# Optimization experiments

Measured on AMD Instinct MI355X. Metric: run time of the kernel, lower is better.

## Reference

```python
import jax, jax.numpy as jnp
import numpy as np


def _layernorm(x, w, b, eps=1e-5):
    mu = x.mean(-1, keepdims=True)
    var = ((x - mu) ** 2).mean(-1, keepdims=True)
    return (x - mu) / jnp.sqrt(var + eps) * w + b


def _conv_res3d(x, w, b):
    # Conv3d(k=3, pad=1) + InstanceNorm3d (no affine) + LeakyReLU(0.01), residual add
    y = jax.lax.conv_general_dilated(x, w, (1, 1, 1), 'SAME',
                                     dimension_numbers=('NCDHW', 'OIDHW', 'NCDHW'))
    y = y + b[None, :, None, None, None]
    mu = y.mean((2, 3, 4), keepdims=True)
    var = ((y - mu) ** 2).mean((2, 3, 4), keepdims=True)
    y = (y - mu) / jnp.sqrt(var + 1e-5)
    y = jnp.where(y >= 0, y, 0.01 * y)
    return x + y


def _ssm(xl, delta_w, delta_b, Bp_w, Cp_w, A_log):
    # xl: [n, l, d_inner]; selective scan with lax.scan over l
    A = -jax.nn.softplus(A_log)                                   # [d_state], broadcast over d_inner
    delta = jnp.clip(jax.nn.softplus(xl @ delta_w.T + delta_b), 1e-4, 10.0)
    Bm = xl @ Bp_w.T                                              # [n, l, d_state]
    Cm = xl @ Cp_w.T
    n, l, di = xl.shape
    ds = A_log.shape[0]

    def step(h, inp):
        d_t, x_t, b_t, c_t = inp                                  # [n,di],[n,di],[n,ds],[n,ds]
        A_bar = jnp.exp(d_t[:, :, None] * A)                      # [n,di,ds]
        h = A_bar * h + (d_t * x_t)[:, :, None] * b_t[:, None, :]
        y = jnp.einsum('nds,ns->nd', h, c_t)
        return h, y

    h0 = jnp.zeros((n, di, ds), xl.dtype)
    _, ys = jax.lax.scan(step, h0, (jnp.swapaxes(delta, 0, 1), jnp.swapaxes(xl, 0, 1),
                                    jnp.swapaxes(Bm, 0, 1), jnp.swapaxes(Cm, 0, 1)))
    return jnp.swapaxes(ys, 0, 1)                                 # [n, l, d_inner]


def _mamba(x, p):
    # x: [n, l, d_model] (already layer-normed)
    left = x @ p['left_w'].T                                      # [n, l, d_inner]
    left = jnp.swapaxes(left, 1, 2)                               # [n, d_inner, l]
    dc = p['conv1d_w'].shape[-1]
    left = jnp.pad(left, ((0, 0), (0, 0), (dc - 1, 0)))           # causal pad
    left = jax.lax.conv_general_dilated(left, p['conv1d_w'], (1,), 'VALID',
                                        feature_group_count=p['conv1d_w'].shape[0],
                                        dimension_numbers=('NCH', 'OIH', 'NCH'))
    left = left + p['conv1d_b'][None, :, None]
    left = jax.nn.silu(jnp.swapaxes(left, 1, 2))                  # [n, l, d_inner]
    y = _ssm(left, p['delta_w'], p['delta_b'], p['Bp_w'], p['Cp_w'], p['A_log'])
    gate = jax.nn.silu(x @ p['right_w'].T)
    out = _layernorm(y * gate, p['pn_w'], p['pn_b'])
    return out @ p['out_w'].T                                     # [n, l, d_model]


def reference(x, cr1_w, cr1_b, cr2_w, cr2_b, ln_w, ln_b, left_w, conv1d_w, conv1d_b,
              delta_w, delta_b, Bp_w, Cp_w, A_log, right_w, pn_w, pn_b, out_w,
              res_scale, axis_w):
    p = dict(left_w=left_w, conv1d_w=conv1d_w, conv1d_b=conv1d_b, delta_w=delta_w,
             delta_b=delta_b, Bp_w=Bp_w, Cp_w=Cp_w, A_log=A_log, right_w=right_w,
             pn_w=pn_w, pn_b=pn_b, out_w=out_w)
    identity = x
    B, C, H, W, D = x.shape
    x = _conv_res3d(x, cr1_w, cr1_b)
    x = _conv_res3d(x, cr2_w, cr2_b)

    xh = jnp.transpose(x, (0, 3, 4, 2, 1)).reshape(B * W * D, H, C)
    mh = _mamba(_layernorm(xh, ln_w, ln_b), p).reshape(B, W, D, H, C).transpose(0, 4, 3, 1, 2)

    xw = jnp.transpose(x, (0, 2, 4, 3, 1)).reshape(B * H * D, W, C)
    mw = _mamba(_layernorm(xw, ln_w, ln_b), p).reshape(B, H, D, W, C).transpose(0, 4, 1, 3, 2)

    xd = jnp.transpose(x, (0, 2, 3, 4, 1)).reshape(B * H * W, D, C)
    md = _mamba(_layernorm(xd, ln_w, ln_b), p).reshape(B, H, W, D, C).transpose(0, 4, 1, 2, 3)

    w = jax.nn.softmax(axis_w)
    out = w[0] * mh + w[1] * mw + w[2] * md
    return identity + res_scale * out


def setup_inputs() -> dict:
    key = jax.random.key(0)
    ks = jax.random.split(key, 12)
    B, C, H, W, D = 2, 64, 32, 32, 32
    ds, dc = 16, 4
    di = 2 * C
    f32 = jnp.float32

    def xav(k, shape):
        fan_in, fan_out = shape[-1], shape[0]
        return jax.random.normal(k, shape, f32) * np.sqrt(2.0 / (fan_in + fan_out))

    return {
        'x': jax.random.normal(ks[0], (B, C, H, W, D), f32),
        'cr1_w': jax.random.normal(ks[1], (C, C, 3, 3, 3), f32) / np.sqrt(C * 27),
        'cr1_b': jnp.zeros((C,), f32),
        'cr2_w': jax.random.normal(ks[2], (C, C, 3, 3, 3), f32) / np.sqrt(C * 27),
        'cr2_b': jnp.zeros((C,), f32),
        'ln_w': jnp.ones((C,), f32),
        'ln_b': jnp.zeros((C,), f32),
        'left_w': xav(ks[3], (di, C)),
        'conv1d_w': jax.random.normal(ks[4], (di, 1, dc), f32) / np.sqrt(dc),
        'conv1d_b': jnp.zeros((di,), f32),
        'delta_w': jax.random.normal(ks[5], (di, di), f32) / np.sqrt(di),
        'delta_b': jnp.zeros((di,), f32),
        'Bp_w': jax.random.normal(ks[6], (ds, di), f32) / np.sqrt(di),
        'Cp_w': jax.random.normal(ks[7], (ds, di), f32) / np.sqrt(di),
        'A_log': jnp.log(jnp.arange(1, ds + 1, dtype=f32)),
        'right_w': xav(ks[8], (di, C)),
        'pn_w': jnp.ones((di,), f32),
        'pn_b': jnp.zeros((di,), f32),
        'out_w': xav(ks[9], (C, di)),
        'res_scale': jnp.asarray(0.1, f32),
        'axis_w': jnp.zeros((3,), f32),
    }
```

## Files before the change

### kernel.cpp

```cpp
#include <hip/hip_runtime.h>
#include <hip/hip_bf16.h>
#include <math.h>
#include <stdint.h>


typedef __attribute__((ext_vector_type(8))) short short8;
typedef __attribute__((ext_vector_type(4))) float f32x4;
typedef __attribute__((ext_vector_type(2))) float f32x2;

__device__ __forceinline__ float siluf(float x){ return x * (1.0f / (1.0f + __expf(-x))); }
__device__ __forceinline__ float softplusf(float x){ return fmaxf(x, 0.0f) + log1pf(__expf(-fabsf(x))); }
__device__ __forceinline__ float softplus_hw(float x){
  float t = __builtin_amdgcn_exp2f(-fabsf(x) * 1.44269504088896f);
  return fmaxf(x, 0.0f) + 0.69314718055995f * __builtin_amdgcn_logf(1.0f + t);
}
__device__ __forceinline__ float b2f(short s){
  unsigned int u = ((unsigned int)(unsigned short)s) << 16;
  float f; __builtin_memcpy(&f, &u, 4); return f;
}
__device__ __forceinline__ short f2b(float v){
  __hip_bfloat16 h = __float2bfloat16(v);
  unsigned short u; __builtin_memcpy(&u, &h, 2); return (short)u;
}
__device__ __forceinline__ f32x2 bf2x(unsigned int u){
  unsigned int lo = u << 16;
  unsigned int hi = u & 0xffff0000u;
  float fl, fh;
  __builtin_memcpy(&fl, &lo, 4);
  __builtin_memcpy(&fh, &hi, 4);
  return (f32x2){fl, fh};
}

__device__ __forceinline__ void gld_lds16(const void* g, void* l){
  __builtin_amdgcn_global_load_lds(
      (__attribute__((address_space(1))) void*)(uintptr_t)g,
      (__attribute__((address_space(3))) void*)(uint32_t)(uintptr_t)l,
      16, 0, 0);
}

__global__ __launch_bounds__(256) void setup_k(uint4* __restrict__ xz,
    const float* __restrict__ cr1w, const float* __restrict__ cr2w,
    const float* __restrict__ lw, const float* __restrict__ rwt,
    const float* __restrict__ dwt, const float* __restrict__ bw,
    const float* __restrict__ cwp, const float* __restrict__ owt,
    const float* __restrict__ alog,
    __hip_bfloat16* __restrict__ W4a, __hip_bfloat16* __restrict__ W4b,
    __hip_bfloat16* __restrict__ Wlr, __hip_bfloat16* __restrict__ Wd,
    __hip_bfloat16* __restrict__ oWp, float* __restrict__ negA2,
    uint4* __restrict__ statz)
{
  int i = blockIdx.x * 256 + threadIdx.x;
  if (i < 628864){ uint4 z; z.x = z.y = z.z = z.w = 0u; xz[i] = z; return; }
  i -= 628864;
  if (i < 110592){
    int tap = i >> 12, co = (i >> 6) & 63, ci = i & 63;
    W4a[i] = __float2bfloat16(cr1w[(co * 64 + ci) * 27 + tap]); return;
  }
  i -= 110592;
  if (i < 110592){
    int tap = i >> 12, co = (i >> 6) & 63, ci = i & 63;
    W4b[i] = __float2bfloat16(cr2w[(co * 64 + ci) * 27 + tap]); return;
  }
  i -= 110592;
  if (i < 16384){
    int row = i >> 6, c = i & 63;
    float v = (row < 128) ? lw[row * 64 + c] : rwt[(row - 128) * 64 + c];
    Wlr[i] = __float2bfloat16(v); return;
  }
  i -= 16384;
  if (i < 20480){
    int row = i >> 7, k = i & 127;
    float v = (row < 128) ? dwt[row * 128 + k]
            : (row < 144 ? bw[(row - 128) * 128 + k] : cwp[(row - 144) * 128 + k]);
    Wd[i] = __float2bfloat16(v); return;
  }
  i -= 20480;
  if (i < 8192){ oWp[i] = __float2bfloat16(owt[i]); return; }
  i -= 8192;
  if (i < 16){ negA2[i] = -softplusf(alog[i]) * 1.44269504088896f; return; }
  i -= 16;
  if (i < 128){ uint4 z; z.x = z.y = z.z = z.w = 0u; statz[i] = z; return; }
}

__global__ __launch_bounds__(256) void pack_k(const float* __restrict__ xin,
                                              __hip_bfloat16* __restrict__ xpad)
{
  __shared__ float lds[64 * 33];
  const int t = threadIdx.x, blk = blockIdx.x;
  const int b = blk >> 10, h = (blk >> 5) & 31, w = blk & 31;
  const size_t rbase = ((size_t)(b * 64) << 15) + h * 1024 + w * 32;
  #pragma unroll
  for (int r = 0; r < 8; r++){
    int c = r * 8 + (t >> 5), d = t & 31;
    lds[c * 33 + d] = xin[rbase + (size_t)c * 32768 + d];
  }
  __syncthreads();
  const size_t wbase = (size_t)b * 2515456 + (size_t)(h + 1) * 73984 + (w + 1) * 2176 + 64;
  #pragma unroll
  for (int r = 0; r < 8; r++){
    int d = r * 4 + (t >> 6), c = t & 63;
    xpad[wbase + d * 64 + c] = __float2bfloat16(lds[c * 33 + d]);
  }
}

__global__ __launch_bounds__(256) void conv_mfma_k(const __hip_bfloat16* __restrict__ xpad,
    const __hip_bfloat16* __restrict__ W4, __hip_bfloat16* __restrict__ y,
    float* __restrict__ stats)
{
  __shared__ short smem[24576];

  const int t = threadIdx.x;
  const int wave = t >> 6, lane = t & 63;
  const int quad = lane >> 4, ln = lane & 15;

  const int blk = blockIdx.x;
  const int xcd = blk & 7, j = blk >> 3;
  const int b = j >> 5, jj = j & 31;
  const int h = xcd * 4 + (jj >> 3);
  const int w0 = (jj & 7) * 4;

  const int bcol = (lane >> 2) * 64 + (lane & 3) * 8;
  const __hip_bfloat16* Bg = xpad + (size_t)b * 2515456 + (size_t)h * 73984
                                  + (size_t)(w0 + wave) * 2176 + bcol;
  const __hip_bfloat16* Ag = W4 + wave * 1024 + bcol;

  f32x4 acc[2][4];
  #pragma unroll
  for (int jn = 0; jn < 2; jn++)
    #pragma unroll
    for (int m = 0; m < 4; m++) acc[jn][m] = (f32x4){0.f, 0.f, 0.f, 0.f};

  const int aoff = ln * 32 + quad * 8;
  const int boffl = wave * 2048 + ln * 32 + quad * 8;

  {
    short* S = &smem[0];
    gld_lds16(Bg,              S + wave * 2048);
    gld_lds16(Bg + 1024,       S + wave * 2048 + 512);
    gld_lds16(Bg + 32,         S + wave * 2048 + 1024);
    gld_lds16(Bg + 1024 + 32,  S + wave * 2048 + 1536);
    gld_lds16(Ag,              S + 8192 + wave * 512);
    gld_lds16(Ag + 32,         S + 8192 + 2048 + wave * 512);
  }
  int cur = 0;
  for (int t1 = 0; t1 < 27; t1++){
    __syncthreads();
    if (t1 + 1 < 27){
      const int t2 = t1 + 1;
      const int ki = t2 / 9, kj = (t2 / 3) % 3, kk = t2 % 3;
      const int tapoff = ki * 73984 + kj * 2176 + kk * 64;
      short* S = &smem[(cur ^ 1) * 12288];
      gld_lds16(Bg + tapoff,             S + wave * 2048);
      gld_lds16(Bg + tapoff + 1024,      S + wave * 2048 + 512);
      gld_lds16(Bg + tapoff + 32,        S + wave * 2048 + 1024);
      gld_lds16(Bg + tapoff + 1024 + 32, S + wave * 2048 + 1536);
      gld_lds16(Ag + t2 * 4096,          S + 8192 + wave * 512);
      gld_lds16(Ag + t2 * 4096 + 32,     S + 8192 + 2048 + wave * 512);
    }
    const int sb = cur * 12288;
    {
      short8 a0 = *(const short8*)&smem[sb + 8192 + aoff];
      short8 a1 = *(const short8*)&smem[sb + 8192 + 512 + aoff];
      short8 a2 = *(const short8*)&smem[sb + 8192 + 1024 + aoff];
      short8 a3 = *(const short8*)&smem[sb + 8192 + 1536 + aoff];
      short8 b0 = *(const short8*)&smem[sb + boffl];
      short8 b1 = *(const short8*)&smem[sb + boffl + 512];
      acc[0][0] = __builtin_amdgcn_mfma_f32_16x16x32_bf16(a0, b0, acc[0][0], 0, 0, 0);
      acc[0][1] = __builtin_amdgcn_mfma_f32_16x16x32_bf16(a1, b0, acc[0][1], 0, 0, 0);
      acc[0][2] = __builtin_amdgcn_mfma_f32_16x16x32_bf16(a2, b0, acc[0][2], 0, 0, 0);
      acc[0][3] = __builtin_amdgcn_mfma_f32_16x16x32_bf16(a3, b0, acc[0][3], 0, 0, 0);
      acc[1][0] = __builtin_amdgcn_mfma_f32_16x16x32_bf16(a0, b1, acc[1][0], 0, 0, 0);
      acc[1][1] = __builtin_amdgcn_mfma_f32_16x16x32_bf16(a1, b1, acc[1][1], 0, 0, 0);
      acc[1][2] = __builtin_amdgcn_mfma_f32_16x16x32_bf16(a2, b1, acc[1][2], 0, 0, 0);
      acc[1][3] = __builtin_amdgcn_mfma_f32_16x16x32_bf16(a3, b1, acc[1][3], 0, 0, 0);
    }
    {
      short8 a0 = *(const short8*)&smem[sb + 8192 + 2048 + aoff];
      short8 a1 = *(const short8*)&smem[sb + 8192 + 2048 + 512 + aoff];
      short8 a2 = *(const short8*)&smem[sb + 8192 + 2048 + 1024 + aoff];
      short8 a3 = *(const short8*)&smem[sb + 8192 + 2048 + 1536 + aoff];
      short8 b0 = *(const short8*)&smem[sb + boffl + 1024];
      short8 b1 = *(const short8*)&smem[sb + boffl + 1536];
      acc[0][0] = __builtin_amdgcn_mfma_f32_16x16x32_bf16(a0, b0, acc[0][0], 0, 0, 0);
      acc[0][1] = __builtin_amdgcn_mfma_f32_16x16x32_bf16(a1, b0, acc[0][1], 0, 0, 0);
      acc[0][2] = __builtin_amdgcn_mfma_f32_16x16x32_bf16(a2, b0, acc[0][2], 0, 0, 0);
      acc[0][3] = __builtin_amdgcn_mfma_f32_16x16x32_bf16(a3, b0, acc[0][3], 0, 0, 0);
      acc[1][0] = __builtin_amdgcn_mfma_f32_16x16x32_bf16(a0, b1, acc[1][0], 0, 0, 0);
      acc[1][1] = __builtin_amdgcn_mfma_f32_16x16x32_bf16(a1, b1, acc[1][1], 0, 0, 0);
      acc[1][2] = __builtin_amdgcn_mfma_f32_16x16x32_bf16(a2, b1, acc[1][2], 0, 0, 0);
      acc[1][3] = __builtin_amdgcn_mfma_f32_16x16x32_bf16(a3, b1, acc[1][3], 0, 0, 0);
    }
    cur ^= 1;
  }

  const size_t sbase = (size_t)h * 1024 + (w0 + wave) * 32 + ln;
  #pragma unroll
  for (int jn = 0; jn < 2; jn++){
    #pragma unroll
    for (int mt = 0; mt < 4; mt++){
      #pragma unroll
      for (int reg = 0; reg < 4; reg++){
        int co = mt * 16 + quad * 4 + reg;
        y[(((size_t)(b * 64 + co)) << 15) + sbase + jn * 16] = __float2bfloat16(acc[jn][mt][reg]);
      }
    }
  }

  __syncthreads();
  float* sred = (float*)smem;
  #pragma unroll
  for (int mt = 0; mt < 4; mt++){
    #pragma unroll
    for (int reg = 0; reg < 4; reg++){
      float a0 = acc[0][mt][reg], a1 = acc[1][mt][reg];
      float s = a0 + a1, s2 = a0 * a0 + a1 * a1;
      #pragma unroll
      for (int m = 1; m < 16; m <<= 1){
        s  += __shfl_xor(s, m);
        s2 += __shfl_xor(s2, m);
      }
      if (ln == 0){
        const int idx = (((wave * 4 + quad) * 4 + mt) * 4 + reg) * 2;
        sred[idx] = s; sred[idx + 1] = s2;
      }
    }
  }
  __syncthreads();
  if (t < 128){
    const int k = t & 1, reg = (t >> 1) & 3, mt = (t >> 3) & 3, q = t >> 5;
    float v = 0.f;
    #pragma unroll
    for (int wv = 0; wv < 4; wv++)
      v += sred[(((wv * 4 + q) * 4 + mt) * 4 + reg) * 2 + k];
    const int co = mt * 16 + q * 4 + reg;
    atomicAdd(&stats[k * 128 + b * 64 + co], v);
  }
}

__global__ __launch_bounds__(256) void apply_pack_k(const float* __restrict__ xin,
    const __hip_bfloat16* __restrict__ y, const float* __restrict__ stats,
    __hip_bfloat16* __restrict__ x1b, __hip_bfloat16* __restrict__ xpad)
{
  __shared__ float lds[64 * 33];
  const int t = threadIdx.x, blk = blockIdx.x;
  const int b = blk >> 10, h = (blk >> 5) & 31, w = blk & 31;
  const size_t rbase = ((size_t)(b * 64) << 15) + h * 1024 + w * 32;
  const int c = t >> 2, d0 = (t & 3) * 8;
  const float s1v = stats[b * 64 + c], s2v = stats[128 + b * 64 + c];
  const float mu = s1v * (1.0f / 32768.0f);
  const float var = s2v * (1.0f / 32768.0f) - mu * mu;
  const float rs = rsqrtf(fmaxf(var, 0.f) + 1e-5f);
  const size_t idx = rbase + (size_t)c * 32768 + d0;
  short8 yv = *(const short8*)&y[idx];
  float4 xa = *(const float4*)&xin[idx];
  float4 xb = *(const float4*)&xin[idx + 4];
  short8 o;
  #pragma unroll
  for (int jj = 0; jj < 8; jj++){
    float v = (b2f(yv[jj]) - mu) * rs;
    v = (v >= 0.0f) ? v : 0.01f * v;
    v += (jj < 4) ? ((const float*)&xa)[jj] : ((const float*)&xb)[jj - 4];
    o[jj] = f2b(v);
    lds[c * 33 + d0 + jj] = v;
  }
  *(short8*)&x1b[idx] = o;
  __syncthreads();
  const size_t wbase = (size_t)b * 2515456 + (size_t)(h + 1) * 73984 + (w + 1) * 2176 + 64;
  #pragma unroll
  for (int r = 0; r < 8; r++){
    int d = r * 4 + (t >> 6), cc = t & 63;
    xpad[wbase + d * 64 + cc] = __float2bfloat16(lds[cc * 33 + d]);
  }
}

__global__ __launch_bounds__(256) void ln_lr_k(const __hip_bfloat16* __restrict__ x1b,
    const __hip_bfloat16* __restrict__ y, const float* __restrict__ stats,
    const float* __restrict__ lnw, const float* __restrict__ lnb,
    const __hip_bfloat16* __restrict__ Wlr, __hip_bfloat16* __restrict__ Lb,
    __hip_bfloat16* __restrict__ Gb)
{
  __shared__ float lds_v[2][64 * 33];
  __shared__ float s_mu[64], s_rs[64];
  __shared__ short s_ln[64 * 68];

  const int t = threadIdx.x, blk = blockIdx.x;
  const int b = blk >> 9;
  const int h = (blk >> 4) & 31;
  const int w0 = (blk & 15) * 2;

  const int c = t >> 2, d0 = (t & 3) * 8;
  const float s1v = stats[b * 64 + c], s2v = stats[128 + b * 64 + c];
  const float mu0 = s1v * (1.0f / 32768.0f);
  const float var0 = s2v * (1.0f / 32768.0f) - mu0 * mu0;
  const float rs0 = rsqrtf(fmaxf(var0, 0.f) + 1e-5f);
  #pragma unroll
  for (int wl = 0; wl < 2; wl++){
    const size_t rbase = ((size_t)(b * 64) << 15) + h * 1024 + (w0 + wl) * 32;
    const size_t idx = rbase + (size_t)c * 32768 + d0;
    short8 yv = *(const short8*)&y[idx];
    short8 xv = *(const short8*)&x1b[idx];
    #pragma unroll
    for (int jj = 0; jj < 8; jj++){
      float v = (b2f(yv[jj]) - mu0) * rs0;
      v = (v >= 0.0f) ? v : 0.01f * v;
      lds_v[wl][c * 33 + d0 + jj] = v + b2f(xv[jj]);
    }
  }
  __syncthreads();

  if (t < 64){
    const int wl = t >> 5, d = t & 31;
    float s = 0.f, s2 = 0.f;
    for (int cc = 0; cc < 64; cc++){
      float v = lds_v[wl][cc * 33 + d];
      s += v; s2 += v * v;
    }
    float mu = s * (1.f / 64.f);
    float var = s2 * (1.f / 64.f) - mu * mu;
    s_mu[t] = mu; s_rs[t] = rsqrtf(var + 1e-5f);
  }
  __syncthreads();

  {
    const int pos_loc = t >> 2, c0 = (t & 3) * 16;
    const int wl = pos_loc >> 5, d = pos_loc & 31;
    const float mu = s_mu[pos_loc], rs = s_rs[pos_loc];
    #pragma unroll
    for (int k = 0; k < 16; k++){
      const int cc = c0 + k;
      s_ln[pos_loc * 68 + cc] = f2b((lds_v[wl][cc * 33 + d] - mu) * rs * lnw[cc] + lnb[cc]);
    }
  }
  __syncthreads();

  const int wave = t >> 6, lane = t & 63, quad = lane >> 4, ln = lane & 15;
  const int pos0 = blk * 64 + wave * 16;
  f32x4 acc[16];
  #pragma unroll
  for (int nt = 0; nt < 16; nt++) acc[nt] = (f32x4){0.f, 0.f, 0.f, 0.f};
  #pragma unroll
  for (int ks = 0; ks < 2; ks++){
    short8 a = *(const short8*)&s_ln[(wave * 16 + ln) * 68 + ks * 32 + quad * 8];
    #pragma unroll
    for (int nt = 0; nt < 16; nt++){
      short8 bv = *(const short8*)&Wlr[(nt * 16 + ln) * 64 + ks * 32 + quad * 8];
      acc[nt] = __builtin_amdgcn_mfma_f32_16x16x32_bf16(a, bv, acc[nt], 0, 0, 0);
    }
  }
  #pragma unroll
  for (int nt = 0; nt < 16; nt++){
    int col = nt * 16 + ln;
    #pragma unroll
    for (int reg = 0; reg < 4; reg++){
      int pos = pos0 + quad * 4 + reg;
      float v = acc[nt][reg];
      if (col < 128) Lb[(size_t)pos * 128 + col] = __float2bfloat16(v);
      else           Gb[(size_t)pos * 128 + col - 128] = __float2bfloat16(siluf(v));
    }
  }
}

__global__ __launch_bounds__(256) void dbcscan_k(const __hip_bfloat16* __restrict__ Lb,
    const float* __restrict__ cw, const float* __restrict__ cb,
    const __hip_bfloat16* __restrict__ Wd, const float* __restrict__ db,
    const __hip_bfloat16* __restrict__ Gb, const float* __restrict__ negA2,
    const float* __restrict__ pnw, const float* __restrict__ pnb,
    const float* __restrict__ axw,
    __hip_bfloat16* __restrict__ Y0, __hip_bfloat16* __restrict__ Y1,
    __hip_bfloat16* __restrict__ Y2)
{
  __shared__ short s_xl[64 * 136];
  __shared__ short s_d[64 * 128];
  __shared__ short s_Bh[2][32][16];
  __shared__ short s_Ch[2][32][16];
  __shared__ float s_stat[2][32][2];

  const int t = threadIdx.x;
  const int bid = blockIdx.x;
  const int axis = bid % 3;
  const int j = bid / 3;
  int sigma;
  if (axis == 0)      sigma = 1024;
  else if (axis == 1) sigma = 32;
  else                sigma = 1;
  __hip_bfloat16* Yax = (axis == 0) ? Y0 : (axis == 1) ? Y1 : Y2;

  int bases[2];
  #pragma unroll
  for (int s = 0; s < 2; s++){
    const int seq = j * 2 + s;
    const int b = seq >> 10, r1 = (seq >> 5) & 31, r0 = seq & 31;
    if (axis == 0)      bases[s] = b * 32768 + r1 * 32 + r0;
    else if (axis == 1) bases[s] = b * 32768 + r1 * 1024 + r0;
    else                bases[s] = b * 32768 + r1 * 1024 + r0 * 32;
  }

  {
    const int c0 = (t & 15) * 8;
    const int pibase = t >> 4;
    float4 w4[8]; float cbv[8];
    #pragma unroll
    for (int c = 0; c < 8; c++){ w4[c] = *(const float4*)&cw[(c0 + c) * 4]; cbv[c] = cb[c0 + c]; }
    #pragma unroll
    for (int r = 0; r < 4; r++){
      const int row = pibase + r * 16;
      const int sl_ = row >> 5, l = row & 31;
      const int pos = bases[sl_] + l * sigma;
      float acc[8];
      #pragma unroll
      for (int c = 0; c < 8; c++) acc[c] = cbv[c];
      #pragma unroll
      for (int jt = 0; jt < 4; jt++){
        const int off = 3 - jt;
        if (l >= off){
          short8 lv = *(const short8*)&Lb[(size_t)(pos - off * sigma) * 128 + c0];
          #pragma unroll
          for (int c = 0; c < 8; c++){
            float wv = (jt == 0) ? w4[c].x : (jt == 1) ? w4[c].y : (jt == 2) ? w4[c].z : w4[c].w;
            acc[c] += wv * b2f(lv[c]);
          }
        }
      }
      short8 o;
      #pragma unroll
      for (int c = 0; c < 8; c++) o[c] = f2b(siluf(acc[c]));
      *(short8*)&s_xl[row * 136 + c0] = o;
    }
  }
  __syncthreads();

  const int wave = t >> 6, lane = t & 63, quad = lane >> 4, ln = lane & 15;
  {
    const int rowb = (wave * 16 + ln) * 136;
    f32x4 acc2[10];
    #pragma unroll
    for (int nt = 0; nt < 10; nt++) acc2[nt] = (f32x4){0.f, 0.f, 0.f, 0.f};
    #pragma unroll
    for (int ks = 0; ks < 4; ks++){
      short8 a = *(const short8*)&s_xl[rowb + ks * 32 + quad * 8];
      #pragma unroll
      for (int nt = 0; nt < 10; nt++){
        short8 bv = *(const short8*)&Wd[(nt * 16 + ln) * 128 + ks * 32 + quad * 8];
        acc2[nt] = __builtin_amdgcn_mfma_f32_16x16x32_bf16(a, bv, acc2[nt], 0, 0, 0);
      }
    }
    const int row0 = wave * 16 + quad * 4;
    #pragma unroll
    for (int nt = 0; nt < 10; nt++){
      const int col = nt * 16 + ln;
      const bool isd = col < 128;
      const float dbv = isd ? db[col] : 0.f;
      #pragma unroll
      for (int reg = 0; reg < 4; reg++){
        const int row = row0 + reg;
        float v = acc2[nt][reg];
        if (isd){
          v = fminf(fmaxf(softplus_hw(v + dbv), 1e-4f), 10.f);
          s_d[row * 128 + col] = f2b(v);
        } else {
          const int sl_ = row >> 5, l = row & 31, cc = col - 128;
          if (cc < 16) s_Bh[sl_][l][cc] = f2b(v);
          else         s_Ch[sl_][l][cc - 16] = f2b(v);
        }
      }
    }
  }

  f32x2 A22[8], h2[8];
  #pragma unroll
  for (int s = 0; s < 8; s++){
    A22[s] = (f32x2){negA2[2 * s], negA2[2 * s + 1]};
    h2[s] = (f32x2){0.f, 0.f};
  }
  const int sl = wave >> 1;
  const int half = wave & 1;
  const int ch = half * 64 + lane;
  const int base = bases[sl];
  const size_t sx = (size_t)sigma * 128;
  const __hip_bfloat16* pg = Gb + (size_t)base * 128 + ch;

  __syncthreads();

  unsigned short gu = *(const unsigned short*)pg;
  #pragma unroll
  for (int l = 0; l < 32; l++){
    unsigned short ngu = 0;
    if (l + 1 < 32) ngu = *(const unsigned short*)(pg + sx);
    const int row = sl * 32 + l;
    float dt = b2f(s_d[row * 128 + ch]);
    float xt = b2f(s_xl[row * 136 + ch]);
    float g = b2f((short)gu);
    float dx = dt * xt;
    const f32x2 dt2 = (f32x2){dt, dt};
    const f32x2 dx2 = (f32x2){dx, dx};
    uint4 Bu0 = *(const uint4*)&s_Bh[sl][l][0];
    uint4 Bu1 = *(const uint4*)&s_Bh[sl][l][8];
    uint4 Cu0 = *(const uint4*)&s_Ch[sl][l][0];
    uint4 Cu1 = *(const uint4*)&s_Ch[sl][l][8];
    const unsigned int Bw[8] = {Bu0.x, Bu0.y, Bu0.z, Bu0.w, Bu1.x, Bu1.y, Bu1.z, Bu1.w};
    const unsigned int Cw[8] = {Cu0.x, Cu0.y, Cu0.z, Cu0.w, Cu1.x, Cu1.y, Cu1.z, Cu1.w};
    f32x2 y2 = (f32x2){0.f, 0.f};
    #pragma unroll
    for (int i = 0; i < 8; i++){
      f32x2 dtA = dt2 * A22[i];
      f32x2 es = (f32x2){__builtin_amdgcn_exp2f(dtA.x),
                         __builtin_amdgcn_exp2f(dtA.y)};
      h2[i] = es * h2[i] + dx2 * bf2x(Bw[i]);
      y2 = y2 + h2[i] * bf2x(Cw[i]);
    }
    float y = y2.x + y2.y;
    s_d[row * 128 + ch] = f2b(y * g);
    gu = ngu;
    pg += sx;
  }
  __syncthreads();

  {
    const int row = t >> 2, part = t & 3;
    const int sl2 = row >> 5, l2 = row & 31;
    const short* yr = &s_d[row * 128 + part * 32];
    float s1 = 0.f, s2 = 0.f;
    #pragma unroll
    for (int i = 0; i < 32; i++){
      float v = b2f(yr[i]);
      s1 += v; s2 += v * v;
    }
    s1 += __shfl_xor(s1, 1); s2 += __shfl_xor(s2, 1);
    s1 += __shfl_xor(s1, 2); s2 += __shfl_xor(s2, 2);
    if (part == 0){ s_stat[sl2][l2][0] = s1; s_stat[sl2][l2][1] = s2; }
  }
  __syncthreads();

  float a0 = axw[0], a1 = axw[1], a2 = axw[2];
  float mxw = fmaxf(a0, fmaxf(a1, a2));
  float e0 = __expf(a0 - mxw), e1 = __expf(a1 - mxw), e2 = __expf(a2 - mxw);
  float wax = ((axis == 0) ? e0 : (axis == 1) ? e1 : e2) / (e0 + e1 + e2);
  const float pw = pnw[ch], pb = pnb[ch];

  __hip_bfloat16* py = Yax + (size_t)base * 128 + ch;
  #pragma unroll
  for (int l = 0; l < 32; l++){
    float ss1 = s_stat[sl][l][0];
    float ss2 = s_stat[sl][l][1];
    float mu = ss1 * (1.f / 128.f);
    float var = ss2 * (1.f / 128.f) - mu * mu;
    float rs = rsqrtf(fmaxf(var, 0.f) + 1e-5f);
    float yv = b2f(s_d[(sl * 32 + l) * 128 + ch]);
    float o = ((yv - mu) * rs * pw + pb) * wax;
    *(unsigned short*)py = (unsigned short)f2b(o);
    py += sx;
  }
}

__global__ __launch_bounds__(256) void gemm_out_k(const __hip_bfloat16* __restrict__ Y0,
    const __hip_bfloat16* __restrict__ Y1, const __hip_bfloat16* __restrict__ Y2,
    const __hip_bfloat16* __restrict__ oW, const float* __restrict__ xres,
    const float* __restrict__ rsc, float* __restrict__ outp)
{
  const int t = threadIdx.x, wave = t >> 6, lane = t & 63, quad = lane >> 4, ln = lane & 15;
  const int pos0 = blockIdx.x * 64 + wave * 16;
  f32x4 acc[4];
  #pragma unroll
  for (int mt = 0; mt < 4; mt++) acc[mt] = (f32x4){0.f, 0.f, 0.f, 0.f};
  #pragma unroll
  for (int ks = 0; ks < 4; ks++){
    const size_t boffs = (size_t)(pos0 + ln) * 128 + ks * 32 + quad * 8;
    short8 bv0 = *(const short8*)&Y0[boffs];
    short8 bv1 = *(const short8*)&Y1[boffs];
    short8 bv2 = *(const short8*)&Y2[boffs];
    #pragma unroll
    for (int mt = 0; mt < 4; mt++){
      short8 a = *(const short8*)&oW[(mt * 16 + ln) * 128 + ks * 32 + quad * 8];
      acc[mt] = __builtin_amdgcn_mfma_f32_16x16x32_bf16(a, bv0, acc[mt], 0, 0, 0);
      acc[mt] = __builtin_amdgcn_mfma_f32_16x16x32_bf16(a, bv1, acc[mt], 0, 0, 0);
      acc[mt] = __builtin_amdgcn_mfma_f32_16x16x32_bf16(a, bv2, acc[mt], 0, 0, 0);
    }
  }
  float rs = rsc[0];
  const int pos = pos0 + ln;
  const int bb = pos >> 15, hwd = pos & 32767;
  #pragma unroll
  for (int mt = 0; mt < 4; mt++){
    #pragma unroll
    for (int reg = 0; reg < 4; reg++){
      int co = mt * 16 + quad * 4 + reg;
      size_t idx = (((size_t)(bb * 64 + co)) << 15) + hwd;
      outp[idx] = xres[idx] + rs * acc[mt][reg];
    }
  }
}

extern "C" void kernel_launch(void* const* d_in, const int* in_sizes, int n_in,
                              void* d_out, int out_size, void* d_ws, size_t ws_size,
                              hipStream_t stream)
{
  const float* x      = (const float*)d_in[0];
  const float* cr1w   = (const float*)d_in[1];
  const float* cr2w   = (const float*)d_in[3];
  const float* ln_w   = (const float*)d_in[5];
  const float* ln_b   = (const float*)d_in[6];
  const float* left_w = (const float*)d_in[7];
  const float* c1dw   = (const float*)d_in[8];
  const float* c1db   = (const float*)d_in[9];
  const float* dw     = (const float*)d_in[10];
  const float* db     = (const float*)d_in[11];
  const float* bpw    = (const float*)d_in[12];
  const float* cpw    = (const float*)d_in[13];
  const float* alog   = (const float*)d_in[14];
  const float* rw     = (const float*)d_in[15];
  const float* pnw    = (const float*)d_in[16];
  const float* pnb    = (const float*)d_in[17];
  const float* ow     = (const float*)d_in[18];
  const float* rsc    = (const float*)d_in[19];
  const float* axw    = (const float*)d_in[20];
  float* out = (float*)d_out;
  float* wsf = (float*)d_ws;

  __hip_bfloat16* ybuf = (__hip_bfloat16*)d_out;
  __hip_bfloat16* x1b  = (__hip_bfloat16*)wsf;
  float* stats1 = wsf + 4194304;
  float* stats2 = wsf + 4194560;
  float* negA2  = wsf + 4194816;
  __hip_bfloat16* W4a  = (__hip_bfloat16*)(wsf + 4195072);
  __hip_bfloat16* W4b  = W4a + 110592;
  __hip_bfloat16* Wlr  = (__hip_bfloat16*)(wsf + 4305664);
  __hip_bfloat16* Wdbc = (__hip_bfloat16*)(wsf + 4313856);
  __hip_bfloat16* oWp  = (__hip_bfloat16*)(wsf + 4324096);
  __hip_bfloat16* xpad = (__hip_bfloat16*)(wsf + 4328192);
  __hip_bfloat16* Lbuf = (__hip_bfloat16*)(wsf + 6843648);
  __hip_bfloat16* Gbuf = (__hip_bfloat16*)(wsf + 11037952);
  __hip_bfloat16* Y0   = (__hip_bfloat16*)wsf;
  __hip_bfloat16* Y1   = (__hip_bfloat16*)(wsf + 15232256);
  __hip_bfloat16* Y2   = (__hip_bfloat16*)(wsf + 19426560);

  setup_k<<<3498, 256, 0, stream>>>((uint4*)xpad, cr1w, cr2w, left_w, rw, dw, bpw, cpw, ow,
                                    alog, W4a, W4b, Wlr, Wdbc, oWp, negA2,
                                    (uint4*)stats1);

  pack_k<<<2048, 256, 0, stream>>>(x, xpad);
  conv_mfma_k<<<512, 256, 0, stream>>>(xpad, W4a, ybuf, stats1);
  apply_pack_k<<<2048, 256, 0, stream>>>(x, ybuf, stats1, x1b, xpad);
  conv_mfma_k<<<512, 256, 0, stream>>>(xpad, W4b, ybuf, stats2);
  ln_lr_k<<<1024, 256, 0, stream>>>(x1b, ybuf, stats2, ln_w, ln_b, Wlr, Lbuf, Gbuf);

  dbcscan_k<<<3072, 256, 0, stream>>>(Lbuf, c1dw, c1db, Wdbc, db, Gbuf, negA2,
                                      pnw, pnb, axw, Y0, Y1, Y2);

  gemm_out_k<<<1024, 256, 0, stream>>>(Y0, Y1, Y2, oWp, x, rsc, out);
}
```

Measured before the change: 389.8 us.

## Halve conv tile width and split output channels across waves

New measurement: 399.7 us. +2.5%, slower.

```diff
diff --git a/kernel.cpp b/kernel.cpp
--- a/kernel.cpp
+++ b/kernel.cpp
@@ -107,7 +107,7 @@
     const __hip_bfloat16* __restrict__ W4, __hip_bfloat16* __restrict__ y,
     float* __restrict__ stats)
 {
-  __shared__ short smem[24576];
+  __shared__ short smem[16384];
 
   const int t = threadIdx.x;
   const int wave = t >> 6, lane = t & 63;
@@ -115,32 +115,41 @@
 
   const int blk = blockIdx.x;
   const int xcd = blk & 7, j = blk >> 3;
-  const int b = j >> 5, jj = j & 31;
-  const int h = xcd * 4 + (jj >> 3);
-  const int w0 = (jj & 7) * 4;
+  const int b = j >> 6, jj = j & 63;
+  const int h = xcd * 4 + (jj >> 4);
+  const int w0 = (jj & 15) * 2;
+
+  const int wl = wave & 1;
+  const int coh = wave >> 1;
 
   const int bcol = (lane >> 2) * 64 + (lane & 3) * 8;
   const __hip_bfloat16* Bg = xpad + (size_t)b * 2515456 + (size_t)h * 73984
-                                  + (size_t)(w0 + wave) * 2176 + bcol;
-  const __hip_bfloat16* Ag = W4 + wave * 1024 + bcol;
-
-  f32x4 acc[2][4];
+                                  + (size_t)(w0 + (wave & 1)) * 2176 + bcol;
+  const __hip_bfloat16* Ag = W4 + (wave >= 2 ? (wave - 2) * 2048 : 0) + bcol;
+
+  f32x4 acc[2][2];
   #pragma unroll
   for (int jn = 0; jn < 2; jn++)
     #pragma unroll
-    for (int m = 0; m < 4; m++) acc[jn][m] = (f32x4){0.f, 0.f, 0.f, 0.f};
+    for (int m = 0; m < 2; m++) acc[jn][m] = (f32x4){0.f, 0.f, 0.f, 0.f};
 
   const int aoff = ln * 32 + quad * 8;
-  const int boffl = wave * 2048 + ln * 32 + quad * 8;
+  const int boff = wl * 2048 + ln * 32 + quad * 8;
 
   {
     short* S = &smem[0];
-    gld_lds16(Bg,              S + wave * 2048);
-    gld_lds16(Bg + 1024,       S + wave * 2048 + 512);
-    gld_lds16(Bg + 32,         S + wave * 2048 + 1024);
-    gld_lds16(Bg + 1024 + 32,  S + wave * 2048 + 1536);
-    gld_lds16(Ag,              S + 8192 + wave * 512);
-    gld_lds16(Ag + 32,         S + 8192 + 2048 + wave * 512);
+    if (wave < 2){
+      gld_lds16(Bg,             S + wave * 2048);
+      gld_lds16(Bg + 1024,      S + wave * 2048 + 512);
+      gld_lds16(Bg + 32,        S + wave * 2048 + 1024);
+      gld_lds16(Bg + 1024 + 32, S + wave * 2048 + 1536);
+    } else {
+      const int d0 = 4096 + (wave - 2) * 1024;
+      gld_lds16(Ag,         S + d0);
+      gld_lds16(Ag + 1024,  S + d0 + 512);
+      gld_lds16(Ag + 32,    S + d0 + 2048);
+      gld_lds16(Ag + 1056,  S + d0 + 2560);
+    }
   }
   int cur = 0;
   for (int t1 = 0; t1 < 27; t1++){
@@ -149,58 +158,52 @@
       const int t2 = t1 + 1;
       const int ki = t2 / 9, kj = (t2 / 3) % 3, kk = t2 % 3;
       const int tapoff = ki * 73984 + kj * 2176 + kk * 64;
-      short* S = &smem[(cur ^ 1) * 12288];
-      gld_lds16(Bg + tapoff,             S + wave * 2048);
-      gld_lds16(Bg + tapoff + 1024,      S + wave * 2048 + 512);
-      gld_lds16(Bg + tapoff + 32,        S + wave * 2048 + 1024);
-      gld_lds16(Bg + tapoff + 1024 + 32, S + wave * 2048 + 1536);
-      gld_lds16(Ag + t2 * 4096,          S + 8192 + wave * 512);
-      gld_lds16(Ag + t2 * 4096 + 32,     S + 8192 + 2048 + wave * 512);
-    }
-    const int sb = cur * 12288;
+      short* S = &smem[(cur ^ 1) * 8192];
+      if (wave < 2){
+        gld_lds16(Bg + tapoff,             S + wave * 2048);
+        gld_lds16(Bg + tapoff + 1024,      S + wave * 2048 + 512);
+        gld_lds16(Bg + tapoff + 32,        S + wave * 2048 + 1024);
+        gld_lds16(Bg + tapoff + 1024 + 32, S + wave * 2048 + 1536);
+      } else {
+        const int d0 = 4096 + (wave - 2) * 1024;
+        gld_lds16(Ag + t2 * 4096,        S + d0);
+        gld_lds16(Ag + t2 * 4096 + 1024, S + d0 + 512);
+        gld_lds16(Ag + t2 * 4096 + 32,   S + d0 + 2048);
+        gld_lds16(Ag + t2 * 4096 + 1056, S + d0 + 2560);
+      }
+    }
+    const int sb = cur * 8192;
     {
-      short8 a0 = *(const short8*)&smem[sb + 8192 + aoff];
-      short8 a1 = *(const short8*)&smem[sb + 8192 + 512 + aoff];
-      short8 a2 = *(const short8*)&smem[sb + 8192 + 1024 + aoff];
-      short8 a3 = *(const short8*)&smem[sb + 8192 + 1536 + aoff];
-      short8 b0 = *(const short8*)&smem[sb + boffl];
-      short8 b1 = *(const short8*)&smem[sb + boffl + 512];
+      short8 a0 = *(const short8*)&smem[sb + 4096 + coh * 1024 + aoff];
+      short8 a1 = *(const short8*)&smem[sb + 4096 + coh * 1024 + 512 + aoff];
+      short8 b0 = *(const short8*)&smem[sb + boff];
+      short8 b1 = *(const short8*)&smem[sb + boff + 512];
       acc[0][0] = __builtin_amdgcn_mfma_f32_16x16x32_bf16(a0, b0, acc[0][0], 0, 0, 0);
       acc[0][1] = __builtin_amdgcn_mfma_f32_16x16x32_bf16(a1, b0, acc[0][1], 0, 0, 0);
-      acc[0][2] = __builtin_amdgcn_mfma_f32_16x16x32_bf16(a2, b0, acc[0][2], 0, 0, 0);
-      acc[0][3] = __builtin_amdgcn_mfma_f32_16x16x32_bf16(a3, b0, acc[0][3], 0, 0, 0);
       acc[1][0] = __builtin_amdgcn_mfma_f32_16x16x32_bf16(a0, b1, acc[1][0], 0, 0, 0);
       acc[1][1] = __builtin_amdgcn_mfma_f32_16x16x32_bf16(a1, b1, acc[1][1], 0, 0, 0);
-      acc[1][2] = __builtin_amdgcn_mfma_f32_16x16x32_bf16(a2, b1, acc[1][2], 0, 0, 0);
-      acc[1][3] = __builtin_amdgcn_mfma_f32_16x16x32_bf16(a3, b1, acc[1][3], 0, 0, 0);
     }
     {
-      short8 a0 = *(const short8*)&smem[sb + 8192 + 2048 + aoff];
-      short8 a1 = *(const short8*)&smem[sb + 8192 + 2048 + 512 + aoff];
-      short8 a2 = *(const short8*)&smem[sb + 8192 + 2048 + 1024 + aoff];
-      short8 a3 = *(const short8*)&smem[sb + 8192 + 2048 + 1536 + aoff];
-      short8 b0 = *(const short8*)&smem[sb + boffl + 1024];
-      short8 b1 = *(const short8*)&smem[sb + boffl + 1536];
+      short8 a0 = *(const short8*)&smem[sb + 4096 + 2048 + coh * 1024 + aoff];
+      short8 a1 = *(const short8*)&smem[sb + 4096 + 2048 + coh * 1024 + 512 + aoff];
+      short8 b0 = *(const short8*)&smem[sb + boff + 1024];
+      short8 b1 = *(const short8*)&smem[sb + boff + 1536];
       acc[0][0] = __builtin_amdgcn_mfma_f32_16x16x32_bf16(a0, b0, acc[0][0], 0, 0, 0);
       acc[0][1] = __builtin_amdgcn_mfma_f32_16x16x32_bf16(a1, b0, acc[0][1], 0, 0, 0);
-      acc[0][2] = __builtin_amdgcn_mfma_f32_16x16x32_bf16(a2, b0, acc[0][2], 0, 0, 0);
-      acc[0][3] = __builtin_amdgcn_mfma_f32_16x16x32_bf16(a3, b0, acc[0][3], 0, 0, 0);
       acc[1][0] = __builtin_amdgcn_mfma_f32_16x16x32_bf16(a0, b1, acc[1][0], 0, 0, 0);
       acc[1][1] = __builtin_amdgcn_mfma_f32_16x16x32_bf16(a1, b1, acc[1][1], 0, 0, 0);
-      acc[1][2] = __builtin_amdgcn_mfma_f32_16x16x32_bf16(a2, b1, acc[1][2], 0, 0, 0);
-      acc[1][3] = __builtin_amdgcn_mfma_f32_16x16x32_bf16(a3, b1, acc[1][3], 0, 0, 0);
     }
     cur ^= 1;
   }
 
-  const size_t sbase = (size_t)h * 1024 + (w0 + wave) * 32 + ln;
+  const size_t sbase = (size_t)h * 1024 + (w0 + wl) * 32 + ln;
   #pragma unroll
   for (int jn = 0; jn < 2; jn++){
     #pragma unroll
-    for (int mt = 0; mt < 4; mt++){
+    for (int mt = 0; mt < 2; mt++){
       #pragma unroll
       for (int reg = 0; reg < 4; reg++){
-        int co = mt * 16 + quad * 4 + reg;
+        int co = coh * 32 + mt * 16 + quad * 4 + reg;
         y[(((size_t)(b * 64 + co)) << 15) + sbase + jn * 16] = __float2bfloat16(acc[jn][mt][reg]);
       }
     }
@@ -209,7 +212,7 @@
   __syncthreads();
   float* sred = (float*)smem;
   #pragma unroll
-  for (int mt = 0; mt < 4; mt++){
+  for (int mt = 0; mt < 2; mt++){
     #pragma unroll
     for (int reg = 0; reg < 4; reg++){
       float a0 = acc[0][mt][reg], a1 = acc[1][mt][reg];
@@ -220,19 +223,22 @@
         s2 += __shfl_xor(s2, m);
       }
       if (ln == 0){
-        const int idx = (((wave * 4 + quad) * 4 + mt) * 4 + reg) * 2;
+        const int idx = (((wave * 4 + quad) * 2 + mt) * 4 + reg) * 2;
         sred[idx] = s; sred[idx + 1] = s2;
       }
     }
   }
   __syncthreads();
   if (t < 128){
-    const int k = t & 1, reg = (t >> 1) & 3, mt = (t >> 3) & 3, q = t >> 5;
+    const int k = t & 1, reg = (t >> 1) & 3, mt = (t >> 3) & 1;
+    const int q = (t >> 4) & 3, ch = t >> 6;
     float v = 0.f;
     #pragma unroll
-    for (int wv = 0; wv < 4; wv++)
-      v += sred[(((wv * 4 + q) * 4 + mt) * 4 + reg) * 2 + k];
-    const int co = mt * 16 + q * 4 + reg;
+    for (int wv = 0; wv < 2; wv++){
+      const int wvi = ch * 2 + wv;
+      v += sred[(((wvi * 4 + q) * 2 + mt) * 4 + reg) * 2 + k];
+    }
+    const int co = ch * 32 + mt * 16 + q * 4 + reg;
     atomicAdd(&stats[k * 128 + b * 64 + co], v);
   }
 }
@@ -638,9 +644,9 @@
                                     (uint4*)stats1);
 
   pack_k<<<2048, 256, 0, stream>>>(x, xpad);
-  conv_mfma_k<<<512, 256, 0, stream>>>(xpad, W4a, ybuf, stats1);
+  conv_mfma_k<<<1024, 256, 0, stream>>>(xpad, W4a, ybuf, stats1);
   apply_pack_k<<<2048, 256, 0, stream>>>(x, ybuf, stats1, x1b, xpad);
-  conv_mfma_k<<<512, 256, 0, stream>>>(xpad, W4b, ybuf, stats2);
+  conv_mfma_k<<<1024, 256, 0, stream>>>(xpad, W4b, ybuf, stats2);
   ln_lr_k<<<1024, 256, 0, stream>>>(x1b, ybuf, stats2, ln_w, ln_b, Wlr, Lbuf, Gbuf);
 
   dbcscan_k<<<3072, 256, 0, stream>>>(Lbuf, c1dw, c1db, Wdbc, db, Gbuf, negA2,
```
